# Optimization experiments

Hardware: AMD Instinct MI355X
Metric: run time of the kernel (lower is better)

## Reference

```python
import jax, jax.numpy as jnp
import numpy as np

N = 8192
DIMS = 128
HID = 64
NEG = -9e15


def setup_inputs() -> dict:
    key = jax.random.key(0)
    k_adj, k_h, k_w1, k_w2 = jax.random.split(key, 4)
    graph_info = (jax.random.uniform(k_adj, (N, N)) < 0.01).astype(jnp.float32)
    h = jax.random.normal(k_h, (N, DIMS), dtype=jnp.float32)
    # xavier-normal-ish init for the 2-layer scoring MLP (dims -> 64 -> 1)
    W1 = jax.random.normal(k_w1, (DIMS, HID), dtype=jnp.float32) * np.sqrt(2.0 / (DIMS + HID))
    b1 = jnp.zeros((HID,), dtype=jnp.float32)
    W2 = jax.random.normal(k_w2, (HID, 1), dtype=jnp.float32) * np.sqrt(2.0 / (HID + 1))
    b2 = jnp.zeros((1,), dtype=jnp.float32)
    return {"graph_info": graph_info, "h": h, "W1": W1, "b1": b1, "W2": W2, "b2": b2}


def reference(graph_info, h, W1, b1, W2, b2):
    # per-node MLP score: e_j for every node j  -> [N, 1]
    e = jnp.dot(jnp.maximum(jnp.dot(h, W1) + b1, 0.0), W2) + b2
    # e.transpose().repeat(N,1): row i sees scores of all columns j -> broadcast [1, N]
    scores = e[:, 0][None, :]
    # mask non-edges with large negative, softmax over neighbors (dim=-1)
    att = jnp.where(graph_info > 0, scores, jnp.float32(NEG))
    att = jax.nn.softmax(att, axis=-1)
    out = jnp.dot(att, h)  # [N, dims] aggregation
    # sum_flag == 1: rescale each row by its degree (diagflat(num) @ h)
    num = jnp.sum(graph_info, axis=-1)  # [N]
    out = num[:, None] * out
    return out
```

## Files before the change

### kernel.cpp

```cpp
#include <hip/hip_runtime.h>
#include <math.h>

#define NN 8192
#define DIMS 128
#define HID 64
#define CAP 192

typedef float f4v __attribute__((ext_vector_type(4)));
typedef float f2v __attribute__((ext_vector_type(2)));
typedef unsigned short u16x8 __attribute__((ext_vector_type(8)));
typedef unsigned long long u64;

__global__ __launch_bounds__(256) void score_kernel(
    const float* __restrict__ h, const float* __restrict__ W1,
    const float* __restrict__ b1, const float* __restrict__ W2,
    const float* __restrict__ b2, float* __restrict__ ee) {
  __shared__ float sW1[DIMS * HID];
  for (int i = threadIdx.x * 4; i < DIMS * HID; i += 1024)
    *(float4*)&sW1[i] = *(const float4*)&W1[i];
  __syncthreads();
  int wv = threadIdx.x >> 6, lane = threadIdx.x & 63;
  int j0 = blockIdx.x * 16 + wv * 4;
  const f4v* h4 = (const f4v*)(h + (size_t)j0 * DIMS);
  float bb = b1[lane];
  float a0 = bb, a1 = bb, a2 = bb, a3 = bb;
#pragma unroll 8
  for (int d4 = 0; d4 < 32; ++d4) {
    f4v v0 = h4[d4], v1 = h4[d4 + 32], v2 = h4[d4 + 64], v3 = h4[d4 + 96];
    float w0 = sW1[(d4 * 4 + 0) * HID + lane];
    float w1 = sW1[(d4 * 4 + 1) * HID + lane];
    float w2c = sW1[(d4 * 4 + 2) * HID + lane];
    float w3 = sW1[(d4 * 4 + 3) * HID + lane];
    a0 = fmaf(v0.x, w0, a0); a0 = fmaf(v0.y, w1, a0); a0 = fmaf(v0.z, w2c, a0); a0 = fmaf(v0.w, w3, a0);
    a1 = fmaf(v1.x, w0, a1); a1 = fmaf(v1.y, w1, a1); a1 = fmaf(v1.z, w2c, a1); a1 = fmaf(v1.w, w3, a1);
    a2 = fmaf(v2.x, w0, a2); a2 = fmaf(v2.y, w1, a2); a2 = fmaf(v2.z, w2c, a2); a2 = fmaf(v2.w, w3, a2);
    a3 = fmaf(v3.x, w0, a3); a3 = fmaf(v3.y, w1, a3); a3 = fmaf(v3.z, w2c, a3); a3 = fmaf(v3.w, w3, a3);
  }
  float w2 = W2[lane];
  float r0 = fmaxf(a0, 0.f) * w2, r1 = fmaxf(a1, 0.f) * w2;
  float r2 = fmaxf(a2, 0.f) * w2, r3 = fmaxf(a3, 0.f) * w2;
#pragma unroll
  for (int off = 32; off > 0; off >>= 1) {
    r0 += __shfl_xor(r0, off, 64);
    r1 += __shfl_xor(r1, off, 64);
    r2 += __shfl_xor(r2, off, 64);
    r3 += __shfl_xor(r3, off, 64);
  }
  if (lane == 0) {
    float bo = b2[0];
    ee[j0]     = expf(r0 + bo);
    ee[j0 + 1] = expf(r1 + bo);
    ee[j0 + 2] = expf(r2 + bo);
    ee[j0 + 3] = expf(r3 + bo);
  }
}

__device__ __forceinline__ unsigned int f2bf(float f) {
  unsigned u = __float_as_uint(f);
  return (u + 0x7fffu + ((u >> 16) & 1u)) >> 16;
}

__global__ __launch_bounds__(256) void gbuild_kernel(
    const float* __restrict__ h, const float* __restrict__ ee,
    unsigned int* __restrict__ g) {
  int i = blockIdx.x * 256 + threadIdx.x;
  int j = i >> 6;
  float eej = ee[j];
  f2v hv = *(const f2v*)(h + (size_t)i * 2);
  unsigned lo = f2bf(hv.x * eej);
  unsigned hi = f2bf(hv.y * eej);
  g[i] = lo | (hi << 16);
}

#define NIBBLE(v)                                                              \
  ((u64)(((__float_as_uint((v).x) >> 29) & 1u) |                               \
         ((__float_as_uint((v).y) >> 28) & 2u) |                               \
         ((__float_as_uint((v).z) >> 27) & 4u) |                               \
         ((__float_as_uint((v).w) >> 26) & 8u)))

__device__ __forceinline__ void gather_batch8(
    const unsigned short* sidx, int q, int cnt,
    const float* __restrict__ ee, const unsigned int* __restrict__ gb,
    float& ax, float& ay, float& z) {
  if (q >= cnt) return;
  u16x8 jv = *(const u16x8*)(sidx + q);
  int j[8];
#pragma unroll
  for (int k = 0; k < 8; ++k) j[k] = (int)jv[k];
  float wv[8];
#pragma unroll
  for (int k = 0; k < 8; ++k) wv[k] = ee[j[k]];
  unsigned hv[8];
#pragma unroll
  for (int k = 0; k < 8; ++k) hv[k] = gb[(size_t)j[k] * 64];
#pragma unroll
  for (int k = 0; k < 8; ++k) {
    bool vld = (q + k < cnt);
    z += vld ? wv[k] : 0.f;
    float gx = __uint_as_float(hv[k] << 16);
    float gy = __uint_as_float(hv[k] & 0xffff0000u);
    ax += vld ? gx : 0.f;
    ay += vld ? gy : 0.f;
  }
}

__global__ __launch_bounds__(256) void pc_kernel(
    const float* __restrict__ graph, const unsigned int* __restrict__ g,
    const float* __restrict__ ee, float* __restrict__ out) {
  __shared__ unsigned short s_idx[4][CAP];
  volatile __shared__ int s_flag[4];
  int w = threadIdx.x >> 6, lane = threadIdx.x & 63;
  int rbase = blockIdx.x * 4;
  if (threadIdx.x < 4) s_flag[threadIdx.x] = 0;
  __syncthreads();

  if (w < 2) {
    u64 lt = (1ull << lane) - 1ull;
#pragma unroll 1
    for (int i = 0; i < 2; ++i) {
      int s = w * 2 + i;
      int row = rbase + s;
      const f4v* g4 = (const f4v*)(graph + (size_t)row * NN) + lane;
      u64 a0 = 0, a1 = 0;
      f4v c0 = g4[0], c1 = g4[64], c2 = g4[128], c3 = g4[192];
#pragma unroll
      for (int t = 0; t < 8; ++t) {
        f4v n0, n1, n2, n3;
        if (t < 7) {
          const f4v* nb2 = g4 + (t * 4 + 4) * 64;
          n0 = nb2[0]; n1 = nb2[64]; n2 = nb2[128]; n3 = nb2[192];
        }
        {
          u64 q0 = NIBBLE(c0), q1 = NIBBLE(c1), q2 = NIBBLE(c2), q3 = NIBBLE(c3);
          int c = t * 4;
          if (c < 16)     a0 |= q0 << (4 * (c & 15));       else a1 |= q0 << (4 * (c & 15));
          if (c + 1 < 16) a0 |= q1 << (4 * ((c + 1) & 15)); else a1 |= q1 << (4 * ((c + 1) & 15));
          if (c + 2 < 16) a0 |= q2 << (4 * ((c + 2) & 15)); else a1 |= q2 << (4 * ((c + 2) & 15));
          if (c + 3 < 16) a0 |= q3 << (4 * ((c + 3) & 15)); else a1 |= q3 << (4 * ((c + 3) & 15));
        }
        if (t < 7) { c0 = n0; c1 = n1; c2 = n2; c3 = n3; }
      }
      int t0 = (int)__popcll(a0), t1 = (int)__popcll(a1);
      int tot = t0 + t1, incl = tot;
#pragma unroll
      for (int d = 1; d < 64; d <<= 1) {
        int vsh = __shfl_up(incl, d, 64);
        if (lane >= d) incl += vsh;
      }
      int base = incl - tot;
      int cnt = __shfl(incl, 63, 64);
      unsigned short* dst = &s_idx[s][0];
      int pidx = base;
      u64 m = a0;
      while (m) {
        int bit = __ffsll(m) - 1;
        int col = ((bit >> 2) << 8) + lane * 4 + (bit & 3);
        if (pidx < CAP) dst[pidx] = (unsigned short)col;
        ++pidx; m &= m - 1;
      }
      m = a1;
      while (m) {
        int bit = __ffsll(m) - 1;
        int col = 4096 + ((bit >> 2) << 8) + lane * 4 + (bit & 3);
        if (pidx < CAP) dst[pidx] = (unsigned short)col;
        ++pidx; m &= m - 1;
      }
      cnt = cnt < CAP ? cnt : CAP;
      __threadfence_block();
      if (lane == 0) s_flag[s] = cnt + 1;
    }
  } else {
    const unsigned int* gb = g + lane;
#pragma unroll 1
    for (int i = 0; i < 2; ++i) {
      int s = (w - 2) * 2 + i;
      int row = rbase + s;
      int f;
      while ((f = s_flag[s]) == 0) __builtin_amdgcn_s_sleep(1);
      __threadfence_block();
      int cnt = f - 1;
      float ax = 0.f, ay = 0.f, z = 0.f;
#pragma unroll 1
      for (int q = 0; q < cnt; q += 8)
        gather_batch8(&s_idx[s][0], q, cnt, ee, gb, ax, ay, z);
      float scale = cnt > 0 ? (float)cnt / z : 0.f;
      f2v o2; o2.x = ax * scale; o2.y = ay * scale;
      *(f2v*)(out + (size_t)row * DIMS + lane * 2) = o2;
    }
  }
}

extern "C" void kernel_launch(void* const* d_in, const int* in_sizes, int n_in,
                              void* d_out, int out_size, void* d_ws, size_t ws_size,
                              hipStream_t stream) {
  const float* graph = (const float*)d_in[0];
  const float* h     = (const float*)d_in[1];
  const float* W1    = (const float*)d_in[2];
  const float* b1    = (const float*)d_in[3];
  const float* W2    = (const float*)d_in[4];
  const float* b2    = (const float*)d_in[5];
  float* out = (float*)d_out;

  float* ee = (float*)d_ws;
  unsigned int* g = (unsigned int*)((char*)d_ws + NN * sizeof(float));

  score_kernel<<<NN / 16, 256, 0, stream>>>(h, W1, b1, W2, b2, ee);
  gbuild_kernel<<<NN * DIMS / 2 / 256, 256, 0, stream>>>(h, ee, g);
  pc_kernel<<<NN / 4, 256, 0, stream>>>(graph, g, ee, out);
}
```

Before: 75.04 us.

## Replace producer/consumer wave split with one wave per row doing scan and gather

The aggregation kernel no longer splits waves into two producers that scan adjacency rows and two consumers that spin on shared-memory flags and gather. Each of the four waves now handles one row end to end: it scans the dense row into a compact index list in shared memory, then gathers and accumulates the neighbour features itself. This removes the flag polling and sleep, and lets all waves issue the bandwidth-heavy adjacency reads at once instead of only half of them. In exchange, a wave can no longer overlap its gather with another wave's scan inside the block, so overlap depends on interleaving across blocks. The output store also becomes nontemporal.

```diff
diff --git a/kernel.cpp b/kernel.cpp
--- a/kernel.cpp
+++ b/kernel.cpp
@@ -104,90 +104,69 @@
   }
 }
 
-__global__ __launch_bounds__(256) void pc_kernel(
+__global__ __launch_bounds__(256) void agg_kernel(
     const float* __restrict__ graph, const unsigned int* __restrict__ g,
     const float* __restrict__ ee, float* __restrict__ out) {
   __shared__ unsigned short s_idx[4][CAP];
-  volatile __shared__ int s_flag[4];
   int w = threadIdx.x >> 6, lane = threadIdx.x & 63;
-  int rbase = blockIdx.x * 4;
-  if (threadIdx.x < 4) s_flag[threadIdx.x] = 0;
-  __syncthreads();
+  int row = blockIdx.x * 4 + w;
+  const f4v* g4 = (const f4v*)(graph + (size_t)row * NN) + lane;
 
-  if (w < 2) {
-    u64 lt = (1ull << lane) - 1ull;
+  u64 a0 = 0, a1 = 0;
+  f4v c0 = g4[0], c1 = g4[64], c2 = g4[128], c3 = g4[192];
+#pragma unroll
+  for (int t = 0; t < 8; ++t) {
+    f4v n0, n1, n2, n3;
+    if (t < 7) {
+      const f4v* nb2 = g4 + (t * 4 + 4) * 64;
+      n0 = nb2[0]; n1 = nb2[64]; n2 = nb2[128]; n3 = nb2[192];
+    }
+    {
+      u64 q0 = NIBBLE(c0), q1 = NIBBLE(c1), q2 = NIBBLE(c2), q3 = NIBBLE(c3);
+      int c = t * 4;
+      if (c < 16)     a0 |= q0 << (4 * (c & 15));       else a1 |= q0 << (4 * (c & 15));
+      if (c + 1 < 16) a0 |= q1 << (4 * ((c + 1) & 15)); else a1 |= q1 << (4 * ((c + 1) & 15));
+      if (c + 2 < 16) a0 |= q2 << (4 * ((c + 2) & 15)); else a1 |= q2 << (4 * ((c + 2) & 15));
+      if (c + 3 < 16) a0 |= q3 << (4 * ((c + 3) & 15)); else a1 |= q3 << (4 * ((c + 3) & 15));
+    }
+    if (t < 7) { c0 = n0; c1 = n1; c2 = n2; c3 = n3; }
+  }
+
+  int t0 = (int)__popcll(a0), t1 = (int)__popcll(a1);
+  int tot = t0 + t1, incl = tot;
+#pragma unroll
+  for (int d = 1; d < 64; d <<= 1) {
+    int vsh = __shfl_up(incl, d, 64);
+    if (lane >= d) incl += vsh;
+  }
+  int base = incl - tot;
+  int count = __shfl(incl, 63, 64);
+  unsigned short* dst = &s_idx[w][0];
+  int pidx = base;
+  u64 m = a0;
+  while (m) {
+    int bit = __ffsll(m) - 1;
+    int col = ((bit >> 2) << 8) + lane * 4 + (bit & 3);
+    if (pidx < CAP) dst[pidx] = (unsigned short)col;
+    ++pidx; m &= m - 1;
+  }
+  m = a1;
+  while (m) {
+    int bit = __ffsll(m) - 1;
+    int col = 4096 + ((bit >> 2) << 8) + lane * 4 + (bit & 3);
+    if (pidx < CAP) dst[pidx] = (unsigned short)col;
+    ++pidx; m &= m - 1;
+  }
+  if (count > CAP) count = CAP;
+
+  const unsigned int* gb = g + lane;
+  float ax = 0.f, ay = 0.f, z = 0.f;
 #pragma unroll 1
-    for (int i = 0; i < 2; ++i) {
-      int s = w * 2 + i;
-      int row = rbase + s;
-      const f4v* g4 = (const f4v*)(graph + (size_t)row * NN) + lane;
-      u64 a0 = 0, a1 = 0;
-      f4v c0 = g4[0], c1 = g4[64], c2 = g4[128], c3 = g4[192];
-#pragma unroll
-      for (int t = 0; t < 8; ++t) {
-        f4v n0, n1, n2, n3;
-        if (t < 7) {
-          const f4v* nb2 = g4 + (t * 4 + 4) * 64;
-          n0 = nb2[0]; n1 = nb2[64]; n2 = nb2[128]; n3 = nb2[192];
-        }
-        {
-          u64 q0 = NIBBLE(c0), q1 = NIBBLE(c1), q2 = NIBBLE(c2), q3 = NIBBLE(c3);
-          int c = t * 4;
-          if (c < 16)     a0 |= q0 << (4 * (c & 15));       else a1 |= q0 << (4 * (c & 15));
-          if (c + 1 < 16) a0 |= q1 << (4 * ((c + 1) & 15)); else a1 |= q1 << (4 * ((c + 1) & 15));
-          if (c + 2 < 16) a0 |= q2 << (4 * ((c + 2) & 15)); else a1 |= q2 << (4 * ((c + 2) & 15));
-          if (c + 3 < 16) a0 |= q3 << (4 * ((c + 3) & 15)); else a1 |= q3 << (4 * ((c + 3) & 15));
-        }
-        if (t < 7) { c0 = n0; c1 = n1; c2 = n2; c3 = n3; }
-      }
-      int t0 = (int)__popcll(a0), t1 = (int)__popcll(a1);
-      int tot = t0 + t1, incl = tot;
-#pragma unroll
-      for (int d = 1; d < 64; d <<= 1) {
-        int vsh = __shfl_up(incl, d, 64);
-        if (lane >= d) incl += vsh;
-      }
-      int base = incl - tot;
-      int cnt = __shfl(incl, 63, 64);
-      unsigned short* dst = &s_idx[s][0];
-      int pidx = base;
-      u64 m = a0;
-      while (m) {
-        int bit = __ffsll(m) - 1;
-        int col = ((bit >> 2) << 8) + lane * 4 + (bit & 3);
-        if (pidx < CAP) dst[pidx] = (unsigned short)col;
-        ++pidx; m &= m - 1;
-      }
-      m = a1;
-      while (m) {
-        int bit = __ffsll(m) - 1;
-        int col = 4096 + ((bit >> 2) << 8) + lane * 4 + (bit & 3);
-        if (pidx < CAP) dst[pidx] = (unsigned short)col;
-        ++pidx; m &= m - 1;
-      }
-      cnt = cnt < CAP ? cnt : CAP;
-      __threadfence_block();
-      if (lane == 0) s_flag[s] = cnt + 1;
-    }
-  } else {
-    const unsigned int* gb = g + lane;
-#pragma unroll 1
-    for (int i = 0; i < 2; ++i) {
-      int s = (w - 2) * 2 + i;
-      int row = rbase + s;
-      int f;
-      while ((f = s_flag[s]) == 0) __builtin_amdgcn_s_sleep(1);
-      __threadfence_block();
-      int cnt = f - 1;
-      float ax = 0.f, ay = 0.f, z = 0.f;
-#pragma unroll 1
-      for (int q = 0; q < cnt; q += 8)
-        gather_batch8(&s_idx[s][0], q, cnt, ee, gb, ax, ay, z);
-      float scale = cnt > 0 ? (float)cnt / z : 0.f;
-      f2v o2; o2.x = ax * scale; o2.y = ay * scale;
-      *(f2v*)(out + (size_t)row * DIMS + lane * 2) = o2;
-    }
-  }
+  for (int q = 0; q < count; q += 8)
+    gather_batch8(dst, q, count, ee, gb, ax, ay, z);
+  float scale = count > 0 ? (float)count / z : 0.f;
+  f2v o2; o2.x = ax * scale; o2.y = ay * scale;
+  __builtin_nontemporal_store(o2, (f2v*)(out + (size_t)row * DIMS + lane * 2));
 }
 
 extern "C" void kernel_launch(void* const* d_in, const int* in_sizes, int n_in,
@@ -206,5 +185,5 @@
 
   score_kernel<<<NN / 16, 256, 0, stream>>>(h, W1, b1, W2, b2, ee);
   gbuild_kernel<<<NN * DIMS / 2 / 256, 256, 0, stream>>>(h, ee, g);
-  pc_kernel<<<NN / 4, 256, 0, stream>>>(graph, g, ee, out);
+  agg_kernel<<<NN / 4, 256, 0, stream>>>(graph, g, ee, out);
 }
```

Measured after the change: 71.64 us. 4.5% less time.
